# Kernel tuning notes

Hardware: AMD Instinct MI355X
Metric: run time of the kernel (lower is better)

## Reference

```python
import jax, jax.numpy as jnp
import numpy as np

B, S, H = 8, 4096, 2048
TOP_K = 32


def setup_inputs() -> dict:
    key = jax.random.key(0)
    k1, k2, k3 = jax.random.split(key, 3)
    base = jax.random.normal(k1, (B, S, H), dtype=jnp.float32)
    batch_weights = jax.random.normal(k2, (B, 1, H), dtype=jnp.float32)
    intervention_positions = jax.random.randint(k3, (B, S), 0, S, dtype=jnp.int32)
    return {"base": base, "intervention_positions": intervention_positions,
            "batch_weights": batch_weights}


def reference(base, intervention_positions, batch_weights):
    # base: [B,S,H]; intervention_positions: [B,S]; batch_weights: [B,1,H]
    b, s, h = base.shape
    bidx = jnp.arange(b)[:, None]                                   # [B,1]
    # gather intervened hidden states: base[b, pos]  -> [B,S,H]
    gathered = jnp.take_along_axis(base, intervention_positions[..., None], axis=1)
    # psi(h) = ReLU(W h): rank-1 bmm with batch_weights -> [B,S]
    detect_latent = jax.nn.relu(
        jnp.einsum('bsh,bh->bs', gathered, batch_weights[:, 0, :]))
    topk_vals, topk_idx = jax.lax.top_k(detect_latent, TOP_K)       # [B,K]
    # zero out the top-k entries (scatter along last dim)
    non_topk_latents = detect_latent.at[bidx, topk_idx].set(0.0)
    # steering vector: mean(topk) * W  -> [B,1,H]
    steer = jnp.mean(topk_vals, axis=-1)[:, None, None] * batch_weights
    # scatter-add steering vector back at the intervened positions
    mixed_output = base.at[bidx, intervention_positions].add(
        jnp.broadcast_to(steer, (b, s, h)))
    return mixed_output, detect_latent, non_topk_latents
```

## Files before the change

### kernel.cpp

```cpp
#include <hip/hip_runtime.h>

#define TOPK 32

typedef float vfloat4 __attribute__((ext_vector_type(4)));

__global__ void hist_kernel(const int* __restrict__ pos,
                            int* __restrict__ counts,
                            int S) {
    extern __shared__ int cnt[];
    int b = blockIdx.x;
    int t = threadIdx.x;
    for (int i = t; i < S; i += 256) cnt[i] = 0;
    __syncthreads();
    for (int i = t; i < S; i += 256)
        atomicAdd(&cnt[pos[(size_t)b * S + i]], 1);
    __syncthreads();
    for (int i = t; i < S; i += 256)
        counts[(size_t)b * S + i] = cnt[i];
}

__global__ void dot_kernel(const float* __restrict__ base,
                           const float* __restrict__ bw,
                           const int* __restrict__ counts,
                           float* __restrict__ d2,
                           int S, int H) {
    int wid  = (blockIdx.x * blockDim.x + threadIdx.x) >> 6;
    int lane = threadIdx.x & 63;
    if (counts[wid] == 0) return;
    int b = wid / S;

    const float4* row = (const float4*)(base + (size_t)wid * H);
    const float4* w4  = (const float4*)(bw + (size_t)b * H);
    int n4 = H >> 2;

    float acc = 0.f;
    #pragma unroll 8
    for (int i = lane; i < n4; i += 64) {
        float4 v = row[i];
        float4 w = w4[i];
        acc += v.x * w.x + v.y * w.y + v.z * w.z + v.w * w.w;
    }
    #pragma unroll
    for (int off = 32; off > 0; off >>= 1)
        acc += __shfl_down(acc, off, 64);

    if (lane == 0) d2[wid] = acc;
}

__global__ void topk_kernel(const float* __restrict__ d2,
                            const int* __restrict__ pos,
                            float* __restrict__ detect,
                            float* __restrict__ nontopk,
                            float* __restrict__ meanv,
                            int S) {
    extern __shared__ float smem[];
    float* dvals = smem;
    float* vals  = smem + S;

    int b = blockIdx.x;
    int t = threadIdx.x;

    for (int i = t; i < S; i += 256)
        dvals[i] = d2[(size_t)b * S + i];
    __syncthreads();
    for (int i = t; i < S; i += 256) {
        float v = fmaxf(dvals[pos[(size_t)b * S + i]], 0.f);
        vals[i] = v;
        detect[(size_t)b * S + i] = v;
    }
    __syncthreads();

    if (t < 64) {
        int lane = t;
        float sum = 0.f;
        for (int it = 0; it < TOPK; ++it) {
            float lv = -INFINITY;
            int   li = 0x7fffffff;
            for (int c = lane * 4; c < S; c += 256) {
                float4 v = *(const float4*)&vals[c];
                if (v.x > lv) { lv = v.x; li = c; }
                if (v.y > lv) { lv = v.y; li = c + 1; }
                if (v.z > lv) { lv = v.z; li = c + 2; }
                if (v.w > lv) { lv = v.w; li = c + 3; }
            }
            #pragma unroll
            for (int off = 32; off > 0; off >>= 1) {
                float ov = __shfl_down(lv, off, 64);
                int   oi = __shfl_down(li, off, 64);
                if (ov > lv || (ov == lv && oi < li)) { lv = ov; li = oi; }
            }
            lv = __shfl(lv, 0, 64);
            li = __shfl(li, 0, 64);
            sum += lv;
            if (lane == 0) vals[li] = -INFINITY;
        }
        if (lane == 0) meanv[b] = sum / (float)TOPK;
    }
    __syncthreads();

    for (int i = t; i < S; i += 256) {
        float v = vals[i];
        nontopk[(size_t)b * S + i] = (v == -INFINITY) ? 0.f : v;
    }
}

__global__ void mix_kernel(const float* __restrict__ base,
                           const float* __restrict__ bw,
                           const int* __restrict__ counts,
                           const float* __restrict__ meanv,
                           float* __restrict__ mixed,
                           int S, int H) {
    int r0 = blockIdx.x << 2;
    int b  = r0 / S;
    const float4* w4 = (const float4*)(bw + (size_t)b * H);
    float mb = meanv[b];
    int n4 = H >> 2;

    for (int r = r0; r < r0 + 4; ++r) {
        float scale = (float)counts[r] * mb;
        const float4* b4 = (const float4*)(base + (size_t)r * H);
        vfloat4*      o4 = (vfloat4*)(mixed + (size_t)r * H);
        #pragma unroll 2
        for (int i = threadIdx.x; i < n4; i += blockDim.x) {
            float4 v = b4[i];
            float4 w = w4[i];
            vfloat4 o;
            o.x = v.x + scale * w.x;
            o.y = v.y + scale * w.y;
            o.z = v.z + scale * w.z;
            o.w = v.w + scale * w.w;
            __builtin_nontemporal_store(o, &o4[i]);
        }
    }
}

extern "C" void kernel_launch(void* const* d_in, const int* in_sizes, int n_in,
                              void* d_out, int out_size, void* d_ws, size_t ws_size,
                              hipStream_t stream) {
    const float* base = (const float*)d_in[0];
    const int*   pos  = (const int*)d_in[1];
    const float* bw   = (const float*)d_in[2];

    long n0 = in_sizes[0];
    long n1 = in_sizes[1];
    long n2 = in_sizes[2];
    int H = (int)(n0 / n1);
    int B = (int)(n2 / H);
    int S = (int)(n1 / B);

    float* out_mixed   = (float*)d_out;
    float* out_detect  = out_mixed + (size_t)B * S * H;
    float* out_nontopk = out_detect + (size_t)B * S;

    int*   counts = (int*)d_ws;
    float* d2     = (float*)((char*)d_ws + (size_t)B * S * sizeof(int));
    float* meanv  = (float*)((char*)d_ws + 2 * (size_t)B * S * sizeof(int));

    int nrows = B * S;
    hist_kernel<<<B, 256, (size_t)S * sizeof(int), stream>>>(pos, counts, S);
    dot_kernel<<<nrows / 4, 256, 0, stream>>>(base, bw, counts, d2, S, H);
    topk_kernel<<<B, 256, 2 * (size_t)S * sizeof(float), stream>>>(
        d2, pos, out_detect, out_nontopk, meanv, S);
    mix_kernel<<<nrows / 4, 256, 0, stream>>>(base, bw, counts, meanv, out_mixed, S, H);
}
```

Baseline: 177.6 us.

## Overlap top-k with copying unintervened rows in a combined kernel

The top-k kernel now runs B selection blocks alongside 1024 extra blocks. The extra blocks copy base rows with zero count straight to the output, and mix_kernel skips those rows. This uses the mostly idle GPU during the serial top-k phase to do part of the output bandwidth work, which shortens the final mix pass. Shared memory becomes a static 8192-float array, which caps S at 4096.

```diff
diff --git a/kernel.cpp b/kernel.cpp
--- a/kernel.cpp
+++ b/kernel.cpp
@@ -47,60 +47,78 @@
     if (lane == 0) d2[wid] = acc;
 }
 
-__global__ void topk_kernel(const float* __restrict__ d2,
-                            const int* __restrict__ pos,
-                            float* __restrict__ detect,
-                            float* __restrict__ nontopk,
-                            float* __restrict__ meanv,
-                            int S) {
-    extern __shared__ float smem[];
-    float* dvals = smem;
-    float* vals  = smem + S;
-
-    int b = blockIdx.x;
+__global__ void topk_copy_kernel(const float* __restrict__ d2,
+                                 const int* __restrict__ pos,
+                                 const int* __restrict__ counts,
+                                 const float* __restrict__ base,
+                                 float* __restrict__ mixed,
+                                 float* __restrict__ detect,
+                                 float* __restrict__ nontopk,
+                                 float* __restrict__ meanv,
+                                 int B, int S, int H, int nblocks) {
+    __shared__ float smem[8192];
     int t = threadIdx.x;
 
-    for (int i = t; i < S; i += 256)
-        dvals[i] = d2[(size_t)b * S + i];
-    __syncthreads();
-    for (int i = t; i < S; i += 256) {
-        float v = fmaxf(dvals[pos[(size_t)b * S + i]], 0.f);
-        vals[i] = v;
-        detect[(size_t)b * S + i] = v;
-    }
-    __syncthreads();
+    if (blockIdx.x < B) {
+        float* dvals = smem;
+        float* vals  = smem + S;
+        int b = blockIdx.x;
 
-    if (t < 64) {
-        int lane = t;
-        float sum = 0.f;
-        for (int it = 0; it < TOPK; ++it) {
-            float lv = -INFINITY;
-            int   li = 0x7fffffff;
-            for (int c = lane * 4; c < S; c += 256) {
-                float4 v = *(const float4*)&vals[c];
-                if (v.x > lv) { lv = v.x; li = c; }
-                if (v.y > lv) { lv = v.y; li = c + 1; }
-                if (v.z > lv) { lv = v.z; li = c + 2; }
-                if (v.w > lv) { lv = v.w; li = c + 3; }
+        for (int i = t; i < S; i += 256)
+            dvals[i] = d2[(size_t)b * S + i];
+        __syncthreads();
+        for (int i = t; i < S; i += 256) {
+            float v = fmaxf(dvals[pos[(size_t)b * S + i]], 0.f);
+            vals[i] = v;
+            detect[(size_t)b * S + i] = v;
+        }
+        __syncthreads();
+
+        if (t < 64) {
+            int lane = t;
+            float sum = 0.f;
+            for (int it = 0; it < TOPK; ++it) {
+                float lv = -INFINITY;
+                int   li = 0x7fffffff;
+                for (int c = lane * 4; c < S; c += 256) {
+                    float4 v = *(const float4*)&vals[c];
+                    if (v.x > lv) { lv = v.x; li = c; }
+                    if (v.y > lv) { lv = v.y; li = c + 1; }
+                    if (v.z > lv) { lv = v.z; li = c + 2; }
+                    if (v.w > lv) { lv = v.w; li = c + 3; }
+                }
+                #pragma unroll
+                for (int off = 32; off > 0; off >>= 1) {
+                    float ov = __shfl_down(lv, off, 64);
+                    int   oi = __shfl_down(li, off, 64);
+                    if (ov > lv || (ov == lv && oi < li)) { lv = ov; li = oi; }
+                }
+                lv = __shfl(lv, 0, 64);
+                li = __shfl(li, 0, 64);
+                sum += lv;
+                if (lane == 0) vals[li] = -INFINITY;
             }
-            #pragma unroll
-            for (int off = 32; off > 0; off >>= 1) {
-                float ov = __shfl_down(lv, off, 64);
-                int   oi = __shfl_down(li, off, 64);
-                if (ov > lv || (ov == lv && oi < li)) { lv = ov; li = oi; }
+            if (lane == 0) meanv[b] = sum / (float)TOPK;
+        }
+        __syncthreads();
+        for (int i = t; i < S; i += 256) {
+            float v = vals[i];
+            nontopk[(size_t)b * S + i] = (v == -INFINITY) ? 0.f : v;
+        }
+    } else {
+        int nrows = B * S;
+        int ncopy = nblocks - B;
+        int n4 = H >> 2;
+        for (int row = blockIdx.x - B; row < nrows; row += ncopy) {
+            if (counts[row] != 0) continue;
+            const vfloat4* bp = (const vfloat4*)(base + (size_t)row * H);
+            vfloat4*       op = (vfloat4*)(mixed + (size_t)row * H);
+            #pragma unroll 2
+            for (int i = t; i < n4; i += 256) {
+                vfloat4 v = __builtin_nontemporal_load(&bp[i]);
+                __builtin_nontemporal_store(v, &op[i]);
             }
-            lv = __shfl(lv, 0, 64);
-            li = __shfl(li, 0, 64);
-            sum += lv;
-            if (lane == 0) vals[li] = -INFINITY;
         }
-        if (lane == 0) meanv[b] = sum / (float)TOPK;
-    }
-    __syncthreads();
-
-    for (int i = t; i < S; i += 256) {
-        float v = vals[i];
-        nontopk[(size_t)b * S + i] = (v == -INFINITY) ? 0.f : v;
     }
 }
 
@@ -117,7 +135,9 @@
     int n4 = H >> 2;
 
     for (int r = r0; r < r0 + 4; ++r) {
-        float scale = (float)counts[r] * mb;
+        int c = counts[r];
+        if (c == 0) continue;
+        float scale = (float)c * mb;
         const float4* b4 = (const float4*)(base + (size_t)r * H);
         vfloat4*      o4 = (vfloat4*)(mixed + (size_t)r * H);
         #pragma unroll 2
@@ -157,9 +177,12 @@
     float* meanv  = (float*)((char*)d_ws + 2 * (size_t)B * S * sizeof(int));
 
     int nrows = B * S;
+    int nk2   = B + 1024;
+
     hist_kernel<<<B, 256, (size_t)S * sizeof(int), stream>>>(pos, counts, S);
     dot_kernel<<<nrows / 4, 256, 0, stream>>>(base, bw, counts, d2, S, H);
-    topk_kernel<<<B, 256, 2 * (size_t)S * sizeof(float), stream>>>(
-        d2, pos, out_detect, out_nontopk, meanv, S);
+    topk_copy_kernel<<<nk2, 256, 0, stream>>>(
+        d2, pos, counts, base, out_mixed, out_detect, out_nontopk, meanv,
+        B, S, H, nk2);
     mix_kernel<<<nrows / 4, 256, 0, stream>>>(base, bw, counts, meanv, out_mixed, S, H);
 }
```

Result: faster. 166.3 us (-6.4%).
